# Optimization experiments

Hardware: AMD Instinct MI355X
Metric: run time of the kernel (lower is better)

## Reference

```python
import jax, jax.numpy as jnp
import numpy as np

B, S, H, L = 4, 2048, 1024, 4
EPS = 1e-5
NEG = -1e9


def setup_inputs() -> dict:
    key = jax.random.key(0)
    ks = jax.random.split(key, 10)
    scale = 1.0 / np.sqrt(H)
    inp = {
        "x": jax.random.normal(ks[0], (B, S, H), dtype=jnp.float32),
        "mask": jnp.ones((B, 1, S), dtype=jnp.int32),
        # stacked per-layer params; torch Linear weight is [out, in]
        "Wq": jax.random.normal(ks[1], (L, H, H), dtype=jnp.float32) * scale,
        "bq": jnp.zeros((L, H), dtype=jnp.float32),
        "Wk": jax.random.normal(ks[2], (L, H, H), dtype=jnp.float32) * scale,
        "bk": jnp.zeros((L, H), dtype=jnp.float32),
        "Wv": jax.random.normal(ks[3], (L, H, H), dtype=jnp.float32) * scale,
        "bv": jnp.zeros((L, H), dtype=jnp.float32),
        "ln_w": jnp.ones((L, H), dtype=jnp.float32),
        "ln_b": jnp.zeros((L, H), dtype=jnp.float32),
    }
    return inp


def _layer(x, mask0, Wq, bq, Wk, bk, Wv, bv, ln_w, ln_b):
    # torch Linear: y = x @ W^T + b
    q = jnp.einsum("bsh,oh->bso", x, Wq) + bq
    k = jnp.einsum("bsh,oh->bso", x, Wk) + bk
    v = jnp.einsum("bsh,oh->bso", x, Wv) + bv
    inv_sqrt_h = jnp.asarray(1.0 / np.sqrt(H), x.dtype)
    scores = jnp.einsum("bsh,bth->bst", q, k) * inv_sqrt_h  # [B,S,S]
    scores = jnp.where(mask0, jnp.asarray(NEG, x.dtype), scores)
    probs = jax.nn.softmax(scores, axis=-1)
    attn = jnp.einsum("bst,bth->bsh", probs, v)
    # residual + LayerNorm (dropout is identity at eval)
    y = x + attn
    mu = jnp.mean(y, axis=-1, keepdims=True)
    var = jnp.mean(jnp.square(y - mu), axis=-1, keepdims=True)
    return ln_w * (y - mu) * jax.lax.rsqrt(var + EPS) + ln_b


def reference(x, mask, Wq, bq, Wk, bk, Wv, bv, ln_w, ln_b):
    mask0 = (mask == 0)  # [B,1,S], broadcasts over query dim
    for l in range(Wq.shape[0]):
        x = _layer(x, mask0, Wq[l], bq[l], Wk[l], bk[l], Wv[l], bv[l], ln_w[l], ln_b[l])
    return x
```

## Files before the change

kernel.cpp:

```cpp
#include <hip/hip_runtime.h>
#include <stdint.h>

typedef __bf16 bf16_t;
typedef __bf16 bf16x8 __attribute__((ext_vector_type(8)));
typedef __bf16 bf16x4 __attribute__((ext_vector_type(4)));
typedef float f32x4 __attribute__((ext_vector_type(4)));
typedef unsigned int u32;

#define DEVINL static __device__ __forceinline__

constexpr int BB = 4;
constexpr int SEQ = 2048;
constexpr int HID = 1024;
constexpr int NL = 4;
constexpr int MR = BB * SEQ;
constexpr float LN_EPS = 1e-5f;
constexpr float MASK_NEG = -1e9f;

DEVINL f32x4 mfma16x16x32(bf16x8 a, bf16x8 b, f32x4 c) {
  return __builtin_amdgcn_mfma_f32_16x16x32_bf16(a, b, c, 0, 0, 0);
}

DEVINL void gload_lds16(const bf16_t* g, bf16_t* l) {
  __builtin_amdgcn_global_load_lds(
      (const __attribute__((address_space(1))) u32*)g,
      (__attribute__((address_space(3))) u32*)l, 16, 0, 0);
}

template <int EPI>
__global__ __launch_bounds__(512, 2) void gemm8(
    const bf16_t* __restrict__ Ab, const bf16_t* __restrict__ B0,
    const bf16_t* __restrict__ B1, const bf16_t* __restrict__ B2,
    const float* __restrict__ bias0, const float* __restrict__ bias1,
    const float* __restrict__ bias2, bf16_t* __restrict__ o0,
    bf16_t* __restrict__ o1, bf16_t* __restrict__ o2) {
  constexpr int TM = (EPI == 0) ? 32 : 8;
  constexpr int TN = (EPI == 1) ? 8 : 4;
  constexpr int LDA = (EPI == 2) ? SEQ : HID;
  constexpr int LDB = (EPI == 2) ? SEQ : HID;
  constexpr int LDC = (EPI == 1) ? SEQ : HID;
  constexpr int NT = 16;

  __shared__ bf16_t lA[2 * 16384];
  __shared__ bf16_t lB[2 * 16384];

  const int nwg = gridDim.x;
  int Lb = blockIdx.x;
  Lb = (Lb & 7) * (nwg >> 3) + (Lb >> 3);
  const int z = Lb / (TM * TN);
  const int rem = Lb - z * (TM * TN);
  const int tm = rem / TN;
  const int tn = rem - tm * TN;
  const int brow = tm * 256, bcol = tn * 256;

  const bf16_t* A;
  const bf16_t* B;
  const float* bias = nullptr;
  bf16_t* outb = nullptr;
  if (EPI == 0) {
    A = Ab;
    B = (z == 0) ? B0 : (z == 1) ? B1 : B2;
    bias = (z == 0) ? bias0 : (z == 1) ? bias1 : bias2;
    outb = (z == 0) ? o0 : (z == 1) ? o1 : o2;
  } else if (EPI == 1) {
    A = Ab + (size_t)z * SEQ * HID;
    B = B0 + (size_t)z * SEQ * HID;
    outb = o0 + (size_t)z * SEQ * SEQ;
  } else {
    const int zb = z >> 1, kh = z & 1;
    A = Ab + (size_t)zb * SEQ * SEQ + kh * 1024;
    B = B0 + (size_t)zb * HID * SEQ + kh * 1024;
    outb = ((kh == 0) ? o0 : o1) + (size_t)zb * SEQ * HID;
  }

  const int t = threadIdx.x, wave = t >> 6, lane = t & 63;
  const int wm = wave >> 2, wn = wave & 3;
  const int fr = lane & 15, kb = lane >> 4;
  const int srow = t >> 3;
  const int cbk = (t & 7) ^ (srow & 7);
  const bf16_t* pAs = A + (size_t)(brow + srow) * LDA + cbk * 8;
  const bf16_t* pBs = B + (size_t)(bcol + srow) * LDB + cbk * 8;
  bf16_t* lAw = lA + wave * 512;
  bf16_t* lBw = lB + wave * 512;

#define SA(X_, h_)                                                       \
  gload_lds16(pAs + (size_t)((h_)*64) * LDA + (X_)*64,                   \
              lAw + ((X_)&1) * 16384 + (h_)*4096)
#define SB(X_, h_)                                                       \
  gload_lds16(pBs + (size_t)((h_)*64) * LDB + (X_)*64,                   \
              lBw + ((X_)&1) * 16384 + (h_)*4096)

  const char* lAc = (const char*)lA;
  const char* lBc = (const char*)lB;
  const int cX0 = ((kb ^ (fr & 7)) << 4);
  const int cX1 = cX0 ^ 64;
  const int bRowOff = (wn & 1) * 64;

  f32x4 acc[8][4] = {};

  SA(0, 0); SA(0, 1); SA(0, 2); SA(0, 3);
  SB(0, 0); SB(0, 1); SB(0, 2); SB(0, 3);
  SA(1, 0); SA(1, 2);
  SB(1, 0); SB(1, 1); SB(1, 2); SB(1, 3);
  asm volatile("s_waitcnt vmcnt(6)" ::: "memory");
  __builtin_amdgcn_s_barrier();

  for (int kt = 0; kt < NT; ++kt) {
    const char* aB = lAc + (size_t)(kt & 1) * 32768 + wm * 16384;
    const char* bB = lBc + (size_t)(kt & 1) * 32768 + (wn >> 1) * 16384;
    bf16x8 bf_[4][2];
#pragma unroll
    for (int p = 0; p < 4; ++p) {
      if (p == 0) {
#pragma unroll
        for (int n = 0; n < 4; ++n) {
          const int rb = (bRowOff + n * 16 + fr) * 128;
          bf_[n][0] = *(const bf16x8*)(bB + rb + cX0);
          bf_[n][1] = *(const bf16x8*)(bB + rb + cX1);
        }
      }
      const int ra0 = (p * 32 + fr) * 128;
      const int ra1 = (p * 32 + 16 + fr) * 128;
      bf16x8 a00 = *(const bf16x8*)(aB + ra0 + cX0);
      bf16x8 a01 = *(const bf16x8*)(aB + ra0 + cX1);
      bf16x8 a10 = *(const bf16x8*)(aB + ra1 + cX0);
      bf16x8 a11 = *(const bf16x8*)(aB + ra1 + cX1);
      if (p == 0 && kt + 1 < NT) { SA(kt + 1, 1); SA(kt + 1, 3); }
      if (p == 1 && kt + 2 < NT) { SB(kt + 2, 0); SB(kt + 2, 1); }
      if (p == 2 && kt + 2 < NT) { SA(kt + 2, 0); SA(kt + 2, 2); }
      if (p == 3 && kt + 2 < NT) { SB(kt + 2, 2); SB(kt + 2, 3); }
      __builtin_amdgcn_s_barrier();
      __builtin_amdgcn_s_setprio(1);
#pragma unroll
      for (int n = 0; n < 4; ++n) {
        acc[2 * p][n] = mfma16x16x32(a00, bf_[n][0], acc[2 * p][n]);
        acc[2 * p][n] = mfma16x16x32(a01, bf_[n][1], acc[2 * p][n]);
        acc[2 * p + 1][n] = mfma16x16x32(a10, bf_[n][0], acc[2 * p + 1][n]);
        acc[2 * p + 1][n] = mfma16x16x32(a11, bf_[n][1], acc[2 * p + 1][n]);
      }
      __builtin_amdgcn_s_setprio(0);
      if (p == 3) {
        if (kt < NT - 3)
          asm volatile("s_waitcnt vmcnt(6)" ::: "memory");
        else
          asm volatile("s_waitcnt vmcnt(0)" ::: "memory");
      }
      __builtin_amdgcn_s_barrier();
    }
  }

  const int qr = lane >> 4;
  const int crow = brow + wm * 128 + qr * 4;
  const int ccol = bcol + wn * 64 + fr;
#pragma unroll
  for (int n = 0; n < 4; ++n) {
    const int col = ccol + n * 16;
    const float badd = (EPI == 0) ? bias[col] : 0.f;
#pragma unroll
    for (int m = 0; m < 8; ++m) {
      const int row = crow + m * 16;
#pragma unroll
      for (int j = 0; j < 4; ++j) {
        const float vv = acc[m][n][j];
        if (EPI == 0)
          outb[(size_t)(row + j) * LDC + col] = (bf16_t)(vv + badd);
        else if (EPI == 1)
          outb[(size_t)(row + j) * LDC + col] = (bf16_t)(vv * 0.03125f);
        else
          outb[(size_t)(row + j) * LDC + col] = (bf16_t)vv;
      }
    }
  }
#undef SA
#undef SB
}

__global__ __launch_bounds__(256) void cast_f32_bf16(
    const float* __restrict__ in, bf16_t* __restrict__ out, long n4) {
  const long stride = (long)gridDim.x * blockDim.x;
  for (long i = (long)blockIdx.x * blockDim.x + threadIdx.x; i < n4;
       i += stride) {
    f32x4 x = *(const f32x4*)(in + i * 4);
    bf16x4 o;
#pragma unroll
    for (int j = 0; j < 4; ++j) o[j] = (bf16_t)x[j];
    *(bf16x4*)(out + i * 4) = o;
  }
}

__global__ __launch_bounds__(256) void transpose_bf16_k(
    const bf16_t* __restrict__ in, bf16_t* __restrict__ out) {
  __shared__ bf16_t tile[64][72];
  const int z = blockIdx.z;
  const bf16_t* src = in + (size_t)z * SEQ * HID;
  bf16_t* dst = out + (size_t)z * SEQ * HID;
  const int r0 = blockIdx.x * 64;
  const int c0 = blockIdx.y * 64;
  const int t = threadIdx.x;
  const int tx = t & 7;
  const int ty = t >> 3;
#pragma unroll
  for (int i = 0; i < 2; ++i) {
    const int r = ty + i * 32;
    bf16x8 vv = *(const bf16x8*)(src + (size_t)(r0 + r) * HID + c0 + tx * 8);
    *(bf16x8*)&tile[r][tx * 8] = vv;
  }
  __syncthreads();
#pragma unroll
  for (int i = 0; i < 2; ++i) {
    const int c = ty + i * 32;
    bf16x8 ov;
#pragma unroll
    for (int j = 0; j < 8; ++j) ov[j] = tile[tx * 8 + j][c];
    *(bf16x8*)(dst + (size_t)(c0 + c) * SEQ + r0 + tx * 8) = ov;
  }
}

__global__ __launch_bounds__(256) void softmax_rows(
    bf16_t* __restrict__ sc, const int* __restrict__ mask) {
  const int row = blockIdx.x;
  const int b = row >> 11;
  bf16_t* p = sc + (size_t)row * SEQ;
  const int* mrow = mask + (size_t)b * SEQ;
  const int t = threadIdx.x;
  const int wave = t >> 6;
  const int lane = t & 63;

  bf16x8 v = *(const bf16x8*)(p + t * 8);
  const int4 m0 = *(const int4*)(mrow + t * 8);
  const int4 m1 = *(const int4*)(mrow + t * 8 + 4);
  const int mk[8] = {m0.x, m0.y, m0.z, m0.w, m1.x, m1.y, m1.z, m1.w};

  float vals[8];
  float mx = -3.4e38f;
#pragma unroll
  for (int j = 0; j < 8; ++j) {
    float s = (float)v[j];
    if (mk[j] == 0) s = MASK_NEG;
    vals[j] = s;
    mx = fmaxf(mx, s);
  }
#pragma unroll
  for (int off = 32; off > 0; off >>= 1)
    mx = fmaxf(mx, __shfl_xor(mx, off, 64));
  __shared__ float red[4];
  if (lane == 0) red[wave] = mx;
  __syncthreads();
  mx = fmaxf(fmaxf(red[0], red[1]), fmaxf(red[2], red[3]));
  __syncthreads();

  float sum = 0.f;
#pragma unroll
  for (int j = 0; j < 8; ++j) {
    vals[j] = __expf(vals[j] - mx);
    sum += vals[j];
  }
#pragma unroll
  for (int off = 32; off > 0; off >>= 1) sum += __shfl_xor(sum, off, 64);
  if (lane == 0) red[wave] = sum;
  __syncthreads();
  sum = red[0] + red[1] + red[2] + red[3];
  const float inv = 1.f / sum;
  bf16x8 o;
#pragma unroll
  for (int j = 0; j < 8; ++j) o[j] = (bf16_t)(vals[j] * inv);
  *(bf16x8*)(p + t * 8) = o;
}

__global__ __launch_bounds__(256) void resid_ln(
    const bf16_t* __restrict__ part0, const bf16_t* __restrict__ part1,
    const float* __restrict__ xin, const float* __restrict__ lnw,
    const float* __restrict__ lnb, float* __restrict__ xout,
    bf16_t* __restrict__ xbout) {
  const int row = blockIdx.x;
  const int t = threadIdx.x;
  const int wave = t >> 6;
  const int lane = t & 63;
  const size_t base = (size_t)row * HID + t * 4;
  const bf16x4 a0 = *(const bf16x4*)(part0 + base);
  const bf16x4 a1 = *(const bf16x4*)(part1 + base);
  const f32x4 xv = *(const f32x4*)(xin + base);
  f32x4 y;
#pragma unroll
  for (int j = 0; j < 4; ++j) y[j] = (float)a0[j] + (float)a1[j] + xv[j];
  float s1 = y[0] + y[1] + y[2] + y[3];
  float s2 = y[0] * y[0] + y[1] * y[1] + y[2] * y[2] + y[3] * y[3];
#pragma unroll
  for (int off = 32; off > 0; off >>= 1) {
    s1 += __shfl_xor(s1, off, 64);
    s2 += __shfl_xor(s2, off, 64);
  }
  __shared__ float red[8];
  if (lane == 0) {
    red[wave] = s1;
    red[4 + wave] = s2;
  }
  __syncthreads();
  s1 = red[0] + red[1] + red[2] + red[3];
  s2 = red[4] + red[5] + red[6] + red[7];
  const float mu = s1 * (1.f / HID);
  const float var = s2 * (1.f / HID) - mu * mu;
  const float rs = rsqrtf(var + LN_EPS);
  const f32x4 wv = *(const f32x4*)(lnw + t * 4);
  const f32x4 bv = *(const f32x4*)(lnb + t * 4);
  f32x4 o;
#pragma unroll
  for (int j = 0; j < 4; ++j) o[j] = wv[j] * ((y[j] - mu) * rs) + bv[j];
  *(f32x4*)(xout + base) = o;
  if (xbout != nullptr) {
    bf16x4 ob;
#pragma unroll
    for (int j = 0; j < 4; ++j) ob[j] = (bf16_t)o[j];
    *(bf16x4*)(xbout + base) = ob;
  }
}

extern "C" void kernel_launch(void* const* d_in, const int* in_sizes, int n_in,
                              void* d_out, int out_size, void* d_ws,
                              size_t ws_size, hipStream_t stream) {
  const float* x_in = (const float*)d_in[0];
  const int* mask = (const int*)d_in[1];
  const float* Wq = (const float*)d_in[2];
  const float* bq = (const float*)d_in[3];
  const float* Wk = (const float*)d_in[4];
  const float* bk = (const float*)d_in[5];
  const float* Wv = (const float*)d_in[6];
  const float* bv = (const float*)d_in[7];
  const float* lnw = (const float*)d_in[8];
  const float* lnb = (const float*)d_in[9];
  float* out = (float*)d_out;

  char* ws = (char*)d_ws;
  size_t off = 0;
  auto alloc = [&](size_t bytes) {
    char* p = ws + off;
    off += (bytes + 255) & ~(size_t)255;
    return (void*)p;
  };
  const size_t LHH = (size_t)NL * HID * HID;
  bf16_t* wqb = (bf16_t*)alloc(LHH * 2);
  bf16_t* wkb = (bf16_t*)alloc(LHH * 2);
  bf16_t* wvb = (bf16_t*)alloc(LHH * 2);
  bf16_t* xb = (bf16_t*)alloc((size_t)MR * HID * 2);
  bf16_t* q = (bf16_t*)alloc((size_t)MR * HID * 2);
  bf16_t* k = (bf16_t*)alloc((size_t)MR * HID * 2);
  bf16_t* v = (bf16_t*)alloc((size_t)MR * HID * 2);
  bf16_t* vT = (bf16_t*)alloc((size_t)MR * HID * 2);
  bf16_t* scores = (bf16_t*)alloc((size_t)BB * SEQ * SEQ * 2);
  bf16_t* attn0 = (bf16_t*)alloc((size_t)MR * HID * 2);
  bf16_t* attn1 = (bf16_t*)alloc((size_t)MR * HID * 2);
  float* xbuf = (float*)alloc((size_t)MR * HID * 4);
  if (off > ws_size) return;

  cast_f32_bf16<<<2048, 256, 0, stream>>>(Wq, wqb, (long)(LHH / 4));
  cast_f32_bf16<<<2048, 256, 0, stream>>>(Wk, wkb, (long)(LHH / 4));
  cast_f32_bf16<<<2048, 256, 0, stream>>>(Wv, wvb, (long)(LHH / 4));
  cast_f32_bf16<<<2048, 256, 0, stream>>>(x_in, xb, (long)((size_t)MR * HID / 4));

  for (int l = 0; l < NL; ++l) {
    const size_t wo = (size_t)l * HID * HID;
    gemm8<0><<<384, 512, 0, stream>>>(xb, wqb + wo, wkb + wo, wvb + wo,
                                      bq + (size_t)l * HID, bk + (size_t)l * HID,
                                      bv + (size_t)l * HID, q, k, v);
    transpose_bf16_k<<<dim3(SEQ / 64, HID / 64, BB), 256, 0, stream>>>(v, vT);
    gemm8<1><<<256, 512, 0, stream>>>(q, k, nullptr, nullptr, nullptr, nullptr,
                                      nullptr, scores, nullptr, nullptr);
    softmax_rows<<<MR, 256, 0, stream>>>(scores, mask);
    gemm8<2><<<256, 512, 0, stream>>>(scores, vT, nullptr, nullptr, nullptr,
                                      nullptr, nullptr, attn0, attn1, nullptr);
    const float* xi = (l == 0) ? x_in : xbuf;
    float* xo = (l == NL - 1) ? out : xbuf;
    bf16_t* xbo = (l == NL - 1) ? nullptr : xb;
    resid_ln<<<MR, 256, 0, stream>>>(attn0, attn1, xi, lnw + (size_t)l * HID,
                                     lnb + (size_t)l * HID, xo, xbo);
  }
}
```

Baseline: 732.0 us.

## Use 256x128 tiles for QKV projection GEMM to double workgroup count

The QKV projection GEMM now uses 256x128 output tiles with a 4x2 wave layout and its own two-phase pipelined K loop, launching 768 workgroups instead of 384. The other two GEMMs keep the original 256x256 path. The aim is better load balance across the CUs, since 384 large tiles fill them unevenly, and a smaller LDS footprint for this GEMM. In exchange, each tile reuses less data, so more global traffic is spent per FLOP.

After: 716.2 us. 1.02x faster.

```diff
diff --git a/kernel.cpp b/kernel.cpp
--- a/kernel.cpp
+++ b/kernel.cpp
@@ -34,24 +34,32 @@
     const float* __restrict__ bias0, const float* __restrict__ bias1,
     const float* __restrict__ bias2, bf16_t* __restrict__ o0,
     bf16_t* __restrict__ o1, bf16_t* __restrict__ o2) {
-  constexpr int TM = (EPI == 0) ? 32 : 8;
-  constexpr int TN = (EPI == 1) ? 8 : 4;
+  constexpr int BM = 256;
+  constexpr int BN = (EPI == 0) ? 128 : 256;
+  constexpr int WN = (EPI == 0) ? 2 : 4;
+  constexpr int WM = 8 / WN;
+  constexpr int MREP = BM / (WM * 16);
+  constexpr int NREP = BN / (WN * 16);
+  constexpr int CA = BM / 64;
+  constexpr int CB = BN / 64;
+  constexpr int TMn = (EPI == 0) ? 32 : 8;
+  constexpr int TNn = (EPI == 0) ? 8 : ((EPI == 1) ? 8 : 4);
   constexpr int LDA = (EPI == 2) ? SEQ : HID;
   constexpr int LDB = (EPI == 2) ? SEQ : HID;
   constexpr int LDC = (EPI == 1) ? SEQ : HID;
   constexpr int NT = 16;
 
-  __shared__ bf16_t lA[2 * 16384];
-  __shared__ bf16_t lB[2 * 16384];
+  __shared__ bf16_t lA[2 * BM * 64];
+  __shared__ bf16_t lB[2 * BN * 64];
 
   const int nwg = gridDim.x;
   int Lb = blockIdx.x;
   Lb = (Lb & 7) * (nwg >> 3) + (Lb >> 3);
-  const int z = Lb / (TM * TN);
-  const int rem = Lb - z * (TM * TN);
-  const int tm = rem / TN;
-  const int tn = rem - tm * TN;
-  const int brow = tm * 256, bcol = tn * 256;
+  const int z = Lb / (TMn * TNn);
+  const int rem = Lb - z * (TMn * TNn);
+  const int tm = rem / TNn;
+  const int tn = rem - tm * TNn;
+  const int brow = tm * BM, bcol = tn * BN;
 
   const bf16_t* A;
   const bf16_t* B;
@@ -74,7 +82,7 @@
   }
 
   const int t = threadIdx.x, wave = t >> 6, lane = t & 63;
-  const int wm = wave >> 2, wn = wave & 3;
+  const int wm = wave / WN, wn = wave % WN;
   const int fr = lane & 15, kb = lane >> 4;
   const int srow = t >> 3;
   const int cbk = (t & 7) ^ (srow & 7);
@@ -83,81 +91,142 @@
   bf16_t* lAw = lA + wave * 512;
   bf16_t* lBw = lB + wave * 512;
 
-#define SA(X_, h_)                                                       \
-  gload_lds16(pAs + (size_t)((h_)*64) * LDA + (X_)*64,                   \
-              lAw + ((X_)&1) * 16384 + (h_)*4096)
-#define SB(X_, h_)                                                       \
-  gload_lds16(pBs + (size_t)((h_)*64) * LDB + (X_)*64,                   \
-              lBw + ((X_)&1) * 16384 + (h_)*4096)
+#define SA(X_, h_)                                                  \
+  gload_lds16(pAs + (size_t)((h_)*64) * LDA + (X_)*64,              \
+              lAw + ((X_)&1) * (BM * 64) + (h_)*4096)
+#define SB(X_, h_)                                                  \
+  gload_lds16(pBs + (size_t)((h_)*64) * LDB + (X_)*64,              \
+              lBw + ((X_)&1) * (BN * 64) + (h_)*4096)
 
   const char* lAc = (const char*)lA;
   const char* lBc = (const char*)lB;
   const int cX0 = ((kb ^ (fr & 7)) << 4);
   const int cX1 = cX0 ^ 64;
-  const int bRowOff = (wn & 1) * 64;
-
-  f32x4 acc[8][4] = {};
-
-  SA(0, 0); SA(0, 1); SA(0, 2); SA(0, 3);
-  SB(0, 0); SB(0, 1); SB(0, 2); SB(0, 3);
-  SA(1, 0); SA(1, 2);
-  SB(1, 0); SB(1, 1); SB(1, 2); SB(1, 3);
-  asm volatile("s_waitcnt vmcnt(6)" ::: "memory");
-  __builtin_amdgcn_s_barrier();
-
-  for (int kt = 0; kt < NT; ++kt) {
-    const char* aB = lAc + (size_t)(kt & 1) * 32768 + wm * 16384;
-    const char* bB = lBc + (size_t)(kt & 1) * 32768 + (wn >> 1) * 16384;
-    bf16x8 bf_[4][2];
-#pragma unroll
-    for (int p = 0; p < 4; ++p) {
-      if (p == 0) {
-#pragma unroll
-        for (int n = 0; n < 4; ++n) {
-          const int rb = (bRowOff + n * 16 + fr) * 128;
-          bf_[n][0] = *(const bf16x8*)(bB + rb + cX0);
-          bf_[n][1] = *(const bf16x8*)(bB + rb + cX1);
-        }
+
+  f32x4 acc[MREP][NREP] = {};
+
+  if constexpr (EPI == 0) {
+    SA(0, 0); SA(0, 1); SA(0, 2); SA(0, 3);
+    SB(0, 0); SB(0, 1);
+    SB(1, 0); SB(1, 1);
+    asm volatile("s_waitcnt vmcnt(2)" ::: "memory");
+    __builtin_amdgcn_s_barrier();
+
+    for (int kt = 0; kt < NT; ++kt) {
+      const char* aB = lAc + (kt & 1) * (BM * 128) + wm * (MREP * 16 * 128);
+      const char* bB = lBc + (kt & 1) * (BN * 128) + wn * (NREP * 16 * 128);
+      bf16x8 bf_[NREP][2];
+#pragma unroll
+      for (int n = 0; n < NREP; ++n) {
+        const int rb = (n * 16 + fr) * 128;
+        bf_[n][0] = *(const bf16x8*)(bB + rb + cX0);
+        bf_[n][1] = *(const bf16x8*)(bB + rb + cX1);
       }
-      const int ra0 = (p * 32 + fr) * 128;
-      const int ra1 = (p * 32 + 16 + fr) * 128;
-      bf16x8 a00 = *(const bf16x8*)(aB + ra0 + cX0);
-      bf16x8 a01 = *(const bf16x8*)(aB + ra0 + cX1);
-      bf16x8 a10 = *(const bf16x8*)(aB + ra1 + cX0);
-      bf16x8 a11 = *(const bf16x8*)(aB + ra1 + cX1);
-      if (p == 0 && kt + 1 < NT) { SA(kt + 1, 1); SA(kt + 1, 3); }
-      if (p == 1 && kt + 2 < NT) { SB(kt + 2, 0); SB(kt + 2, 1); }
-      if (p == 2 && kt + 2 < NT) { SA(kt + 2, 0); SA(kt + 2, 2); }
-      if (p == 3 && kt + 2 < NT) { SB(kt + 2, 2); SB(kt + 2, 3); }
+      bf16x8 a0[2][2];
+#pragma unroll
+      for (int m = 0; m < 2; ++m) {
+        const int ra = (m * 16 + fr) * 128;
+        a0[m][0] = *(const bf16x8*)(aB + ra + cX0);
+        a0[m][1] = *(const bf16x8*)(aB + ra + cX1);
+      }
+      if (kt + 1 < NT) { SA(kt + 1, 0); SA(kt + 1, 1); SA(kt + 1, 2); SA(kt + 1, 3); }
       __builtin_amdgcn_s_barrier();
       __builtin_amdgcn_s_setprio(1);
 #pragma unroll
-      for (int n = 0; n < 4; ++n) {
-        acc[2 * p][n] = mfma16x16x32(a00, bf_[n][0], acc[2 * p][n]);
-        acc[2 * p][n] = mfma16x16x32(a01, bf_[n][1], acc[2 * p][n]);
-        acc[2 * p + 1][n] = mfma16x16x32(a10, bf_[n][0], acc[2 * p + 1][n]);
-        acc[2 * p + 1][n] = mfma16x16x32(a11, bf_[n][1], acc[2 * p + 1][n]);
+      for (int m = 0; m < 2; ++m)
+#pragma unroll
+        for (int n = 0; n < NREP; ++n) {
+          acc[m][n] = mfma16x16x32(a0[m][0], bf_[n][0], acc[m][n]);
+          acc[m][n] = mfma16x16x32(a0[m][1], bf_[n][1], acc[m][n]);
+        }
+      __builtin_amdgcn_s_setprio(0);
+      __builtin_amdgcn_s_barrier();
+      bf16x8 a1[2][2];
+#pragma unroll
+      for (int m = 0; m < 2; ++m) {
+        const int ra = ((m + 2) * 16 + fr) * 128;
+        a1[m][0] = *(const bf16x8*)(aB + ra + cX0);
+        a1[m][1] = *(const bf16x8*)(aB + ra + cX1);
       }
+      if (kt + 2 < NT) { SB(kt + 2, 0); SB(kt + 2, 1); }
+      __builtin_amdgcn_s_barrier();
+      __builtin_amdgcn_s_setprio(1);
+#pragma unroll
+      for (int m = 0; m < 2; ++m)
+#pragma unroll
+        for (int n = 0; n < NREP; ++n) {
+          acc[m + 2][n] = mfma16x16x32(a1[m][0], bf_[n][0], acc[m + 2][n]);
+          acc[m + 2][n] = mfma16x16x32(a1[m][1], bf_[n][1], acc[m + 2][n]);
+        }
       __builtin_amdgcn_s_setprio(0);
-      if (p == 3) {
-        if (kt < NT - 3)
-          asm volatile("s_waitcnt vmcnt(6)" ::: "memory");
-        else
-          asm volatile("s_waitcnt vmcnt(0)" ::: "memory");
-      }
+      if (kt < NT - 2)
+        asm volatile("s_waitcnt vmcnt(2)" ::: "memory");
+      else
+        asm volatile("s_waitcnt vmcnt(0)" ::: "memory");
       __builtin_amdgcn_s_barrier();
     }
+  } else {
+    SA(0, 0); SA(0, 1); SA(0, 2); SA(0, 3);
+    SB(0, 0); SB(0, 1); SB(0, 2); SB(0, 3);
+    SA(1, 0); SA(1, 2);
+    SB(1, 0); SB(1, 1); SB(1, 2); SB(1, 3);
+    asm volatile("s_waitcnt vmcnt(6)" ::: "memory");
+    __builtin_amdgcn_s_barrier();
+
+    for (int kt = 0; kt < NT; ++kt) {
+      const char* aB = lAc + (kt & 1) * (BM * 128) + wm * (MREP * 16 * 128);
+      const char* bB = lBc + (kt & 1) * (BN * 128) + wn * (NREP * 16 * 128);
+      bf16x8 bf_[NREP][2];
+#pragma unroll
+      for (int p = 0; p < 4; ++p) {
+        if (p == 0) {
+#pragma unroll
+          for (int n = 0; n < NREP; ++n) {
+            const int rb = (n * 16 + fr) * 128;
+            bf_[n][0] = *(const bf16x8*)(bB + rb + cX0);
+            bf_[n][1] = *(const bf16x8*)(bB + rb + cX1);
+          }
+        }
+        const int ra0 = (p * 32 + fr) * 128;
+        const int ra1 = (p * 32 + 16 + fr) * 128;
+        bf16x8 a00 = *(const bf16x8*)(aB + ra0 + cX0);
+        bf16x8 a01 = *(const bf16x8*)(aB + ra0 + cX1);
+        bf16x8 a10 = *(const bf16x8*)(aB + ra1 + cX0);
+        bf16x8 a11 = *(const bf16x8*)(aB + ra1 + cX1);
+        if (p == 0 && kt + 1 < NT) { SA(kt + 1, 1); SA(kt + 1, 3); }
+        if (p == 1 && kt + 2 < NT) { SB(kt + 2, 0); SB(kt + 2, 1); }
+        if (p == 2 && kt + 2 < NT) { SA(kt + 2, 0); SA(kt + 2, 2); }
+        if (p == 3 && kt + 2 < NT) { SB(kt + 2, 2); SB(kt + 2, 3); }
+        __builtin_amdgcn_s_barrier();
+        __builtin_amdgcn_s_setprio(1);
+#pragma unroll
+        for (int n = 0; n < NREP; ++n) {
+          acc[2 * p][n] = mfma16x16x32(a00, bf_[n][0], acc[2 * p][n]);
+          acc[2 * p][n] = mfma16x16x32(a01, bf_[n][1], acc[2 * p][n]);
+          acc[2 * p + 1][n] = mfma16x16x32(a10, bf_[n][0], acc[2 * p + 1][n]);
+          acc[2 * p + 1][n] = mfma16x16x32(a11, bf_[n][1], acc[2 * p + 1][n]);
+        }
+        __builtin_amdgcn_s_setprio(0);
+        if (p == 3) {
+          if (kt < NT - 3)
+            asm volatile("s_waitcnt vmcnt(6)" ::: "memory");
+          else
+            asm volatile("s_waitcnt vmcnt(0)" ::: "memory");
+        }
+        __builtin_amdgcn_s_barrier();
+      }
+    }
   }
 
   const int qr = lane >> 4;
-  const int crow = brow + wm * 128 + qr * 4;
-  const int ccol = bcol + wn * 64 + fr;
-#pragma unroll
-  for (int n = 0; n < 4; ++n) {
+  const int crow = brow + wm * (MREP * 16) + qr * 4;
+  const int ccol = bcol + wn * (NREP * 16) + fr;
+#pragma unroll
+  for (int n = 0; n < NREP; ++n) {
     const int col = ccol + n * 16;
     const float badd = (EPI == 0) ? bias[col] : 0.f;
 #pragma unroll
-    for (int m = 0; m < 8; ++m) {
+    for (int m = 0; m < MREP; ++m) {
       const int row = crow + m * 16;
 #pragma unroll
       for (int j = 0; j < 4; ++j) {
@@ -359,7 +428,7 @@
 
   for (int l = 0; l < NL; ++l) {
     const size_t wo = (size_t)l * HID * HID;
-    gemm8<0><<<384, 512, 0, stream>>>(xb, wqb + wo, wkb + wo, wvb + wo,
+    gemm8<0><<<768, 512, 0, stream>>>(xb, wqb + wo, wkb + wo, wvb + wo,
                                       bq + (size_t)l * HID, bk + (size_t)l * HID,
                                       bv + (size_t)l * HID, q, k, v);
     transpose_bf16_k<<<dim3(SEQ / 64, HID / 64, BB), 256, 0, stream>>>(v, vT);
```

## Switch GEMMs to 32x32x16 MFMA with 256x128 block tiles

Applied to the files above, without the earlier changes.

Replaces the 16x16x32 MFMA GEMM with the 32x32x16 bf16 MFMA instruction and shrinks the block tile from 256x256 to 256x128. Each wave now computes a 64x64 output region with four 32x32 accumulators, and the grid doubles in size. The load/compute pipeline is rescheduled around two half-steps per k-tile. The goal is fewer LDS fragment reads per FLOP and more workgroups to fill the CUs. In exchange, each block reuses less data, which means more global traffic for the A operand.

After: 766.6 us. 1.05x slower.

```diff
diff --git a/kernel.cpp b/kernel.cpp
--- a/kernel.cpp
+++ b/kernel.cpp
@@ -5,6 +5,7 @@
 typedef __bf16 bf16x8 __attribute__((ext_vector_type(8)));
 typedef __bf16 bf16x4 __attribute__((ext_vector_type(4)));
 typedef float f32x4 __attribute__((ext_vector_type(4)));
+typedef float f32x16 __attribute__((ext_vector_type(16)));
 typedef unsigned int u32;
 
 #define DEVINL static __device__ __forceinline__
@@ -17,8 +18,8 @@
 constexpr float LN_EPS = 1e-5f;
 constexpr float MASK_NEG = -1e9f;
 
-DEVINL f32x4 mfma16x16x32(bf16x8 a, bf16x8 b, f32x4 c) {
-  return __builtin_amdgcn_mfma_f32_16x16x32_bf16(a, b, c, 0, 0, 0);
+DEVINL f32x16 mfma32(bf16x8 a, bf16x8 b, f32x16 c) {
+  return __builtin_amdgcn_mfma_f32_32x32x16_bf16(a, b, c, 0, 0, 0);
 }
 
 DEVINL void gload_lds16(const bf16_t* g, bf16_t* l) {
@@ -28,30 +29,31 @@
 }
 
 template <int EPI>
-__global__ __launch_bounds__(512, 2) void gemm8(
+__global__ __launch_bounds__(512, 2) void gemm32(
     const bf16_t* __restrict__ Ab, const bf16_t* __restrict__ B0,
     const bf16_t* __restrict__ B1, const bf16_t* __restrict__ B2,
     const float* __restrict__ bias0, const float* __restrict__ bias1,
     const float* __restrict__ bias2, bf16_t* __restrict__ o0,
     bf16_t* __restrict__ o1, bf16_t* __restrict__ o2) {
-  constexpr int TM = (EPI == 0) ? 32 : 8;
-  constexpr int TN = (EPI == 1) ? 8 : 4;
+  constexpr int BM = 256, BN = 128;
+  constexpr int TMn = (EPI == 0) ? (MR / 256) : (SEQ / 256);
+  constexpr int TNn = (EPI == 1) ? (SEQ / 128) : (HID / 128);
   constexpr int LDA = (EPI == 2) ? SEQ : HID;
   constexpr int LDB = (EPI == 2) ? SEQ : HID;
   constexpr int LDC = (EPI == 1) ? SEQ : HID;
   constexpr int NT = 16;
 
-  __shared__ bf16_t lA[2 * 16384];
-  __shared__ bf16_t lB[2 * 16384];
+  __shared__ bf16_t lA[2 * BM * 64];
+  __shared__ bf16_t lB[2 * BN * 64];
 
   const int nwg = gridDim.x;
   int Lb = blockIdx.x;
   Lb = (Lb & 7) * (nwg >> 3) + (Lb >> 3);
-  const int z = Lb / (TM * TN);
-  const int rem = Lb - z * (TM * TN);
-  const int tm = rem / TN;
-  const int tn = rem - tm * TN;
-  const int brow = tm * 256, bcol = tn * 256;
+  const int z = Lb / (TMn * TNn);
+  const int rem = Lb - z * (TMn * TNn);
+  const int tm = rem / TNn;
+  const int tn = rem - tm * TNn;
+  const int brow = tm * BM, bcol = tn * BN;
 
   const bf16_t* A;
   const bf16_t* B;
@@ -74,8 +76,8 @@
   }
 
   const int t = threadIdx.x, wave = t >> 6, lane = t & 63;
-  const int wm = wave >> 2, wn = wave & 3;
-  const int fr = lane & 15, kb = lane >> 4;
+  const int wm = wave >> 1, wn = wave & 1;
+  const int r31 = lane & 31, kb2 = lane >> 5;
   const int srow = t >> 3;
   const int cbk = (t & 7) ^ (srow & 7);
   const bf16_t* pAs = A + (size_t)(brow + srow) * LDA + cbk * 8;
@@ -83,91 +85,91 @@
   bf16_t* lAw = lA + wave * 512;
   bf16_t* lBw = lB + wave * 512;
 
-#define SA(X_, h_)                                                       \
-  gload_lds16(pAs + (size_t)((h_)*64) * LDA + (X_)*64,                   \
-              lAw + ((X_)&1) * 16384 + (h_)*4096)
-#define SB(X_, h_)                                                       \
-  gload_lds16(pBs + (size_t)((h_)*64) * LDB + (X_)*64,                   \
-              lBw + ((X_)&1) * 16384 + (h_)*4096)
+#define SA(X_, h_)                                                  \
+  gload_lds16(pAs + (size_t)((h_)*64) * LDA + (X_)*64,              \
+              lAw + ((X_)&1) * (BM * 64) + (h_)*4096)
+#define SB(X_, h_)                                                  \
+  gload_lds16(pBs + (size_t)((h_)*64) * LDB + (X_)*64,              \
+              lBw + ((X_)&1) * (BN * 64) + (h_)*4096)
 
   const char* lAc = (const char*)lA;
   const char* lBc = (const char*)lB;
-  const int cX0 = ((kb ^ (fr & 7)) << 4);
-  const int cX1 = cX0 ^ 64;
-  const int bRowOff = (wn & 1) * 64;
-
-  f32x4 acc[8][4] = {};
+  int sX[4];
+#pragma unroll
+  for (int ks = 0; ks < 4; ++ks) sX[ks] = (((ks * 2 + kb2) ^ (r31 & 7)) << 4);
+  const int rowA0 = wm * 64 + r31;
+  const int rowB0 = wn * 64 + r31;
+
+  f32x16 acc00 = {}, acc01 = {}, acc10 = {}, acc11 = {};
 
   SA(0, 0); SA(0, 1); SA(0, 2); SA(0, 3);
-  SB(0, 0); SB(0, 1); SB(0, 2); SB(0, 3);
-  SA(1, 0); SA(1, 2);
-  SB(1, 0); SB(1, 1); SB(1, 2); SB(1, 3);
-  asm volatile("s_waitcnt vmcnt(6)" ::: "memory");
+  SB(0, 0); SB(0, 1);
+  SB(1, 0); SB(1, 1);
+  asm volatile("s_waitcnt vmcnt(2)" ::: "memory");
   __builtin_amdgcn_s_barrier();
 
   for (int kt = 0; kt < NT; ++kt) {
-    const char* aB = lAc + (size_t)(kt & 1) * 32768 + wm * 16384;
-    const char* bB = lBc + (size_t)(kt & 1) * 32768 + (wn >> 1) * 16384;
-    bf16x8 bf_[4][2];
-#pragma unroll
-    for (int p = 0; p < 4; ++p) {
-      if (p == 0) {
-#pragma unroll
-        for (int n = 0; n < 4; ++n) {
-          const int rb = (bRowOff + n * 16 + fr) * 128;
-          bf_[n][0] = *(const bf16x8*)(bB + rb + cX0);
-          bf_[n][1] = *(const bf16x8*)(bB + rb + cX1);
-        }
-      }
-      const int ra0 = (p * 32 + fr) * 128;
-      const int ra1 = (p * 32 + 16 + fr) * 128;
-      bf16x8 a00 = *(const bf16x8*)(aB + ra0 + cX0);
-      bf16x8 a01 = *(const bf16x8*)(aB + ra0 + cX1);
-      bf16x8 a10 = *(const bf16x8*)(aB + ra1 + cX0);
-      bf16x8 a11 = *(const bf16x8*)(aB + ra1 + cX1);
-      if (p == 0 && kt + 1 < NT) { SA(kt + 1, 1); SA(kt + 1, 3); }
-      if (p == 1 && kt + 2 < NT) { SB(kt + 2, 0); SB(kt + 2, 1); }
-      if (p == 2 && kt + 2 < NT) { SA(kt + 2, 0); SA(kt + 2, 2); }
-      if (p == 3 && kt + 2 < NT) { SB(kt + 2, 2); SB(kt + 2, 3); }
-      __builtin_amdgcn_s_barrier();
-      __builtin_amdgcn_s_setprio(1);
-#pragma unroll
-      for (int n = 0; n < 4; ++n) {
-        acc[2 * p][n] = mfma16x16x32(a00, bf_[n][0], acc[2 * p][n]);
-        acc[2 * p][n] = mfma16x16x32(a01, bf_[n][1], acc[2 * p][n]);
-        acc[2 * p + 1][n] = mfma16x16x32(a10, bf_[n][0], acc[2 * p + 1][n]);
-        acc[2 * p + 1][n] = mfma16x16x32(a11, bf_[n][1], acc[2 * p + 1][n]);
-      }
-      __builtin_amdgcn_s_setprio(0);
-      if (p == 3) {
-        if (kt < NT - 3)
-          asm volatile("s_waitcnt vmcnt(6)" ::: "memory");
+    const char* aB = lAc + (kt & 1) * (BM * 128);
+    const char* bB = lBc + (kt & 1) * (BN * 128);
+    bf16x8 bF[2][4], a0[4];
+#pragma unroll
+    for (int ni = 0; ni < 2; ++ni)
+#pragma unroll
+      for (int ks = 0; ks < 4; ++ks)
+        bF[ni][ks] = *(const bf16x8*)(bB + (rowB0 + ni * 32) * 128 + sX[ks]);
+#pragma unroll
+    for (int ks = 0; ks < 4; ++ks)
+      a0[ks] = *(const bf16x8*)(aB + rowA0 * 128 + sX[ks]);
+    if (kt + 1 < NT) { SA(kt + 1, 0); SA(kt + 1, 1); SA(kt + 1, 2); SA(kt + 1, 3); }
+    __builtin_amdgcn_s_barrier();
+    __builtin_amdgcn_s_setprio(1);
+#pragma unroll
+    for (int ks = 0; ks < 4; ++ks) {
+      acc00 = mfma32(a0[ks], bF[0][ks], acc00);
+      acc01 = mfma32(a0[ks], bF[1][ks], acc01);
+    }
+    __builtin_amdgcn_s_setprio(0);
+    __builtin_amdgcn_s_barrier();
+    bf16x8 a1[4];
+#pragma unroll
+    for (int ks = 0; ks < 4; ++ks)
+      a1[ks] = *(const bf16x8*)(aB + (rowA0 + 32) * 128 + sX[ks]);
+    if (kt + 2 < NT) { SB(kt + 2, 0); SB(kt + 2, 1); }
+    __builtin_amdgcn_s_barrier();
+    __builtin_amdgcn_s_setprio(1);
+#pragma unroll
+    for (int ks = 0; ks < 4; ++ks) {
+      acc10 = mfma32(a1[ks], bF[0][ks], acc10);
+      acc11 = mfma32(a1[ks], bF[1][ks], acc11);
+    }
+    __builtin_amdgcn_s_setprio(0);
+    if (kt < NT - 2)
+      asm volatile("s_waitcnt vmcnt(2)" ::: "memory");
+    else
+      asm volatile("s_waitcnt vmcnt(0)" ::: "memory");
+    __builtin_amdgcn_s_barrier();
+  }
+
+  const int crow = brow + wm * 64 + 4 * kb2;
+  const int ccol = bcol + wn * 64 + r31;
+#pragma unroll
+  for (int mi = 0; mi < 2; ++mi) {
+#pragma unroll
+    for (int ni = 0; ni < 2; ++ni) {
+      const f32x16 av = (mi == 0) ? (ni == 0 ? acc00 : acc01)
+                                  : (ni == 0 ? acc10 : acc11);
+      const int col = ccol + ni * 32;
+      const float badd = (EPI == 0) ? bias[col] : 0.f;
+#pragma unroll
+      for (int r = 0; r < 16; ++r) {
+        const int row = crow + mi * 32 + (r & 3) + 8 * (r >> 2);
+        const float vv = av[r];
+        if (EPI == 0)
+          outb[(size_t)row * LDC + col] = (bf16_t)(vv + badd);
+        else if (EPI == 1)
+          outb[(size_t)row * LDC + col] = (bf16_t)(vv * 0.03125f);
         else
-          asm volatile("s_waitcnt vmcnt(0)" ::: "memory");
-      }
-      __builtin_amdgcn_s_barrier();
-    }
-  }
-
-  const int qr = lane >> 4;
-  const int crow = brow + wm * 128 + qr * 4;
-  const int ccol = bcol + wn * 64 + fr;
-#pragma unroll
-  for (int n = 0; n < 4; ++n) {
-    const int col = ccol + n * 16;
-    const float badd = (EPI == 0) ? bias[col] : 0.f;
-#pragma unroll
-    for (int m = 0; m < 8; ++m) {
-      const int row = crow + m * 16;
-#pragma unroll
-      for (int j = 0; j < 4; ++j) {
-        const float vv = acc[m][n][j];
-        if (EPI == 0)
-          outb[(size_t)(row + j) * LDC + col] = (bf16_t)(vv + badd);
-        else if (EPI == 1)
-          outb[(size_t)(row + j) * LDC + col] = (bf16_t)(vv * 0.03125f);
-        else
-          outb[(size_t)(row + j) * LDC + col] = (bf16_t)vv;
+          outb[(size_t)row * LDC + col] = (bf16_t)vv;
       }
     }
   }
@@ -359,15 +361,15 @@
 
   for (int l = 0; l < NL; ++l) {
     const size_t wo = (size_t)l * HID * HID;
-    gemm8<0><<<384, 512, 0, stream>>>(xb, wqb + wo, wkb + wo, wvb + wo,
-                                      bq + (size_t)l * HID, bk + (size_t)l * HID,
-                                      bv + (size_t)l * HID, q, k, v);
+    gemm32<0><<<768, 512, 0, stream>>>(xb, wqb + wo, wkb + wo, wvb + wo,
+                                       bq + (size_t)l * HID, bk + (size_t)l * HID,
+                                       bv + (size_t)l * HID, q, k, v);
     transpose_bf16_k<<<dim3(SEQ / 64, HID / 64, BB), 256, 0, stream>>>(v, vT);
-    gemm8<1><<<256, 512, 0, stream>>>(q, k, nullptr, nullptr, nullptr, nullptr,
-                                      nullptr, scores, nullptr, nullptr);
+    gemm32<1><<<512, 512, 0, stream>>>(q, k, nullptr, nullptr, nullptr, nullptr,
+                                       nullptr, scores, nullptr, nullptr);
     softmax_rows<<<MR, 256, 0, stream>>>(scores, mask);
-    gemm8<2><<<256, 512, 0, stream>>>(scores, vT, nullptr, nullptr, nullptr,
-                                      nullptr, nullptr, attn0, attn1, nullptr);
+    gemm32<2><<<512, 512, 0, stream>>>(scores, vT, nullptr, nullptr, nullptr,
+                                       nullptr, nullptr, attn0, attn1, nullptr);
     const float* xi = (l == 0) ? x_in : xbuf;
     float* xo = (l == NL - 1) ? out : xbuf;
     bf16_t* xbo = (l == NL - 1) ? nullptr : xb;
```
